# Performance work log

Hardware: AMD Instinct MI355X
Metric: run time of the kernel (lower is better)

Reference implementation:

```python
import jax, jax.numpy as jnp
import numpy as np

B, S, C = 8, 2048, 512

def setup_inputs() -> dict:
    key = jax.random.key(0)
    ks = jax.random.split(key, 7)
    s = 1.0 / np.sqrt(C)
    return {
        "x": jax.random.normal(ks[0], (B, S, C), dtype=jnp.float32),
        "Wq": jax.random.uniform(ks[1], (C, C), jnp.float32, -s, s),
        "bq": jax.random.uniform(ks[2], (C,), jnp.float32, -s, s),
        "Wk": jax.random.uniform(ks[3], (C, C), jnp.float32, -s, s),
        "bk": jax.random.uniform(ks[4], (C,), jnp.float32, -s, s),
        "Wv": jax.random.uniform(ks[5], (C, C), jnp.float32, -s, s),
        "bv": jax.random.uniform(ks[6], (C,), jnp.float32, -s, s),
    }

def reference(x, Wq, bq, Wk, bk, Wv, bv):
    # Linear projections (torch Linear: x @ W.T + b)
    q = jnp.einsum('bsc,dc->bsd', x, Wq) + bq
    k = jnp.einsum('bsc,dc->bsd', x, Wk) + bk
    v = jnp.einsum('bsc,dc->bsd', x, Wv) + bv
    # NOTE: original code computes dk but never scales by 1/sqrt(dk)
    scores = jnp.einsum('bqd,bkd->bqk', q, k)          # [B,S,S]
    attn = jax.nn.softmax(scores, axis=-1)
    out = jnp.einsum('bqk,bkd->bqd', attn, v)
    return out + x
```

## Files before the change

### kernel.cpp

```cpp
#include <hip/hip_runtime.h>
#include <hip/hip_bf16.h>


typedef __bf16 bf16_t;
typedef bf16_t bf16x8 __attribute__((ext_vector_type(8)));
typedef float floatx4 __attribute__((ext_vector_type(4)));

#define MFMA16(a, b, c) __builtin_amdgcn_mfma_f32_16x16x32_bf16((a), (b), (c), 0, 0, 0)
#define FLASH_LDS 140800

__device__ __forceinline__ void gload16(const void* g, void* l) {
    __builtin_amdgcn_global_load_lds((const __attribute__((address_space(1))) void*)g,
                                     (__attribute__((address_space(3))) void*)l, 16, 0, 0);
}

__device__ __forceinline__ float wave16_sum(float v) {
    v += __shfl_xor(v, 1);
    v += __shfl_xor(v, 2);
    v += __shfl_xor(v, 4);
    v += __shfl_xor(v, 8);
    return v;
}

__global__ void convert_in(const float* __restrict__ X,
                           const float* __restrict__ Wq, const float* __restrict__ Wk,
                           const float* __restrict__ Wv, const float* __restrict__ bq,
                           const float* __restrict__ bk, const float* __restrict__ bv,
                           bf16_t* __restrict__ Xb, bf16_t* __restrict__ Wb,
                           float* __restrict__ biasc) {
    int bid = blockIdx.x, tid = threadIdx.x;
    if (bid < 4096) {
        size_t e0 = ((size_t)bid * 256 + tid) * 8;
        float4 f0 = *(const float4*)(X + e0);
        float4 f1 = *(const float4*)(X + e0 + 4);
        bf16x8 o;
        o[0] = (bf16_t)f0.x; o[1] = (bf16_t)f0.y; o[2] = (bf16_t)f0.z; o[3] = (bf16_t)f0.w;
        o[4] = (bf16_t)f1.x; o[5] = (bf16_t)f1.y; o[6] = (bf16_t)f1.z; o[7] = (bf16_t)f1.w;
        *(bf16x8*)(Xb + e0) = o;
    } else {
        int idx = (bid - 4096) * 256 + tid;
        int e0 = idx * 4;
        int row = e0 >> 9, c = e0 & 511;
        const float* src;
        if (row < 512)       src = Wq + row * 512;
        else if (row < 1024) src = Wk + (row - 512) * 512;
        else                 src = Wv + (row - 1024) * 512;
        float4 v = *(const float4*)(src + c);
        Wb[e0 + 0] = (bf16_t)v.x;
        Wb[e0 + 1] = (bf16_t)v.y;
        Wb[e0 + 2] = (bf16_t)v.z;
        Wb[e0 + 3] = (bf16_t)v.w;
        if (idx < 1536) {
            float b;
            if (idx < 512)       b = bq[idx];
            else if (idx < 1024) b = bk[idx - 512];
            else                 b = bv[idx - 1024];
            biasc[idx] = b;
        }
    }
}

__global__ __launch_bounds__(256, 2)
void qkv_gemm(const bf16_t* __restrict__ Xb, const bf16_t* __restrict__ Wb,
              const float* __restrict__ biasc, bf16_t* __restrict__ Q,
              bf16_t* __restrict__ K, bf16_t* __restrict__ Vt) {
    __shared__ int4 smem4[2560];
    char* As = (char*)smem4;
    char* Bs = (char*)smem4 + 16384;
    char* Vtile = (char*)smem4;

    const int tid = threadIdx.x;
    const int l = tid & 63, w = tid >> 6;
    const int lane16 = l & 15, lq = l >> 4;
    const int klo = lane16 & 7;
    const int m0 = (blockIdx.x & 127) << 7;
    const int n0 = (blockIdx.x >> 7) << 7;
    const int wm = (w >> 1) << 6, wn = (w & 1) << 6;
    const int srow = l >> 3;
    const int sc8 = (l & 7) ^ srow;

    floatx4 acc[4][4];
#pragma unroll
    for (int a = 0; a < 4; ++a)
#pragma unroll
        for (int bb = 0; bb < 4; ++bb) acc[a][bb] = (floatx4){0.f, 0.f, 0.f, 0.f};

    for (int it = 0; it < 8; ++it) {
        __syncthreads();
#pragma unroll
        for (int j = 0; j < 4; ++j) {
            int seg = j * 4 + w;
            int row = seg * 8 + srow;
            gload16(Xb + (size_t)(m0 + row) * 512 + it * 64 + sc8 * 8, As + seg * 1024);
            gload16(Wb + (size_t)(n0 + row) * 512 + it * 64 + sc8 * 8, Bs + seg * 1024);
        }
        __syncthreads();
#pragma unroll
        for (int kst = 0; kst < 2; ++kst) {
            bf16x8 afr[4], bfr[4];
#pragma unroll
            for (int mt = 0; mt < 4; ++mt)
                afr[mt] = *(const bf16x8*)(As + (wm + mt * 16 + lane16) * 128 +
                                           ((kst * 4 + lq) ^ klo) * 16);
#pragma unroll
            for (int nt = 0; nt < 4; ++nt)
                bfr[nt] = *(const bf16x8*)(Bs + (wn + nt * 16 + lane16) * 128 +
                                           ((kst * 4 + lq) ^ klo) * 16);
#pragma unroll
            for (int mt = 0; mt < 4; ++mt)
#pragma unroll
                for (int nt = 0; nt < 4; ++nt)
                    acc[mt][nt] = MFMA16(afr[mt], bfr[nt], acc[mt][nt]);
        }
    }

    float bias_v[4];
#pragma unroll
    for (int nt = 0; nt < 4; ++nt) bias_v[nt] = biasc[n0 + wn + nt * 16 + lane16];

    if (n0 < 1024) {
        bf16_t* Dst = (n0 < 512) ? Q : K;
        const int coff = (n0 < 512 ? n0 : n0 - 512) + wn;
#pragma unroll
        for (int mt = 0; mt < 4; ++mt)
#pragma unroll
            for (int nt = 0; nt < 4; ++nt)
#pragma unroll
                for (int i = 0; i < 4; ++i) {
                    int rowM = m0 + wm + mt * 16 + lq * 4 + i;
                    Dst[(size_t)rowM * 512 + coff + nt * 16 + lane16] =
                        (bf16_t)(acc[mt][nt][i] + bias_v[nt]);
                }
    } else {
        __syncthreads();
#pragma unroll
        for (int mt = 0; mt < 4; ++mt)
#pragma unroll
            for (int nt = 0; nt < 4; ++nt)
#pragma unroll
                for (int i = 0; i < 4; ++i) {
                    int dl = wn + nt * 16 + lane16;
                    int sl = wm + mt * 16 + lq * 4 + i;
                    *(bf16_t*)(Vtile + dl * 264 + sl * 2) =
                        (bf16_t)(acc[mt][nt][i] + bias_v[nt]);
                }
        __syncthreads();
        const int bb = m0 >> 11, s0 = m0 & 2047, dbase = n0 - 1024;
#pragma unroll
        for (int j = 0; j < 8; ++j) {
            int slot = j * 256 + tid;
            int dd = slot >> 4, c = slot & 15;
            *(int4*)(Vt + (size_t)(bb * 512 + dbase + dd) * 2048 + s0 + c * 8) =
                *(const int4*)(Vtile + dd * 264 + c * 16);
        }
    }
}

__global__ __launch_bounds__(512, 2)
void flash_attn_v3(const bf16_t* __restrict__ Q, const bf16_t* __restrict__ K,
                   const bf16_t* __restrict__ Vt, const float* __restrict__ X,
                   float* __restrict__ Out) {
    extern __shared__ char smem[];
    char* Ks = smem;
    char* Vs = smem + 65536;
    char* Ps = smem + 131072;
    float* lpart = (float*)(smem + 140288);

    const int tid = threadIdx.x;
    const int l = tid & 63, w = tid >> 6;
    const int lane16 = l & 15, lq = l >> 4;
    const int qg = w >> 1, h = w & 1;
    const int dbase = w << 6;
    const int b = blockIdx.x & 7;
    const int q0 = (blockIdx.x >> 3) << 6;

    const bf16_t* Kbase = K + (size_t)b * 2048 * 512;
    const bf16_t* Vbase = Vt + (size_t)b * 512 * 2048;

#pragma unroll
    for (int j = 0; j < 8; ++j) {
        int seg = j * 8 + w;
        int c = (l & ~7) | ((l & 7) ^ (seg & 7));
        gload16(Kbase + (size_t)seg * 512 + c * 8, Ks + seg * 1024);
    }

    bf16x8 qf[16];
    const bf16_t* Qrow = Q + (size_t)(b * 2048 + q0 + qg * 16 + lane16) * 512 + lq * 8;
#pragma unroll
    for (int kst = 0; kst < 16; ++kst) qf[kst] = *(const bf16x8*)(Qrow + kst * 32);

    floatx4 o[16];
#pragma unroll
    for (int t = 0; t < 16; ++t) o[t] = (floatx4){0.f, 0.f, 0.f, 0.f};
    float lsum[4] = {0.f, 0.f, 0.f, 0.f};
    const float L2E = 1.4426950408889634f;

    __syncthreads();

    for (int kt = 0; kt < 32; ++kt) {
        {
            const bf16_t* Vsrc = Vbase + kt * 64;
#pragma unroll
            for (int j = 0; j < 8; ++j) {
                int seg = j * 8 + w;
                int d = seg * 8 + (l >> 3);
                int c = (l & 7) ^ (l >> 3);
                gload16(Vsrc + (size_t)d * 2048 + c * 8, Vs + seg * 1024);
            }
        }
        floatx4 scA[2], scB[2];
#pragma unroll
        for (int g = 0; g < 2; ++g) {
            scA[g] = (floatx4){0.f, 0.f, 0.f, 0.f};
            scB[g] = (floatx4){0.f, 0.f, 0.f, 0.f};
        }
#pragma unroll
        for (int kst = 0; kst < 16; kst += 2) {
#pragma unroll
            for (int g = 0; g < 2; ++g) {
                int key = h * 32 + g * 16 + lane16;
                int i0 = kst * 4 + lq;
                int i1 = i0 + 4;
                int p0 = (i0 & ~7) | ((i0 & 7) ^ (key & 7));
                int p1 = (i1 & ~7) | ((i1 & 7) ^ (key & 7));
                bf16x8 kb0 = *(const bf16x8*)(Ks + key * 1024 + p0 * 16);
                bf16x8 kb1 = *(const bf16x8*)(Ks + key * 1024 + p1 * 16);
                scA[g] = MFMA16(qf[kst], kb0, scA[g]);
                scB[g] = MFMA16(qf[kst + 1], kb1, scB[g]);
            }
        }
#pragma unroll
        for (int g = 0; g < 2; ++g) {
            int keyc = h * 32 + g * 16 + lane16;
#pragma unroll
            for (int i = 0; i < 4; ++i) {
                float p = __builtin_exp2f((scA[g][i] + scB[g][i]) * L2E);
                lsum[i] += p;
                *(bf16_t*)(Ps + (qg * 16 + lq * 4 + i) * 144 + keyc * 2) = (bf16_t)p;
            }
        }
        __syncthreads();

        if (kt < 31) {
            const bf16_t* Ksrc = Kbase + (size_t)(kt + 1) * 64 * 512;
#pragma unroll
            for (int j = 0; j < 8; ++j) {
                int seg = j * 8 + w;
                int c = (l & ~7) | ((l & 7) ^ (seg & 7));
                gload16(Ksrc + (size_t)seg * 512 + c * 8, Ks + seg * 1024);
            }
        }
#pragma unroll
        for (int kk = 0; kk < 2; ++kk) {
            bf16x8 pa[4];
#pragma unroll
            for (int qgi = 0; qgi < 4; ++qgi)
                pa[qgi] = *(const bf16x8*)(Ps + (qgi * 16 + lane16) * 144 + kk * 64 + lq * 16);
#pragma unroll
            for (int dg = 0; dg < 4; ++dg) {
                int d = dbase + dg * 16 + lane16;
                int pos = (kk * 4 + lq) ^ (d & 7);
                bf16x8 vb = *(const bf16x8*)(Vs + d * 128 + pos * 16);
#pragma unroll
                for (int qgi = 0; qgi < 4; ++qgi)
                    o[qgi * 4 + dg] = MFMA16(pa[qgi], vb, o[qgi * 4 + dg]);
            }
        }
        __syncthreads();
    }

#pragma unroll
    for (int i = 0; i < 4; ++i) {
        float s = wave16_sum(lsum[i]);
        if (lane16 == 0) lpart[(qg * 16 + lq * 4 + i) * 2 + h] = s;
    }
    __syncthreads();

#pragma unroll
    for (int qgi = 0; qgi < 4; ++qgi) {
        float rinv[4];
#pragma unroll
        for (int i = 0; i < 4; ++i) {
            int row = qgi * 16 + lq * 4 + i;
            rinv[i] = 1.0f / (lpart[row * 2] + lpart[row * 2 + 1]);
        }
#pragma unroll
        for (int dg = 0; dg < 4; ++dg) {
            int d = dbase + dg * 16 + lane16;
#pragma unroll
            for (int i = 0; i < 4; ++i) {
                int row = q0 + qgi * 16 + lq * 4 + i;
                size_t g = (size_t)(b * 2048 + row) * 512 + d;
                Out[g] = o[qgi * 4 + dg][i] * rinv[i] + X[g];
            }
        }
    }
}

extern "C" void kernel_launch(void* const* d_in, const int* in_sizes, int n_in,
                              void* d_out, int out_size, void* d_ws, size_t ws_size,
                              hipStream_t stream) {
    const float* x  = (const float*)d_in[0];
    const float* Wq = (const float*)d_in[1];
    const float* bq = (const float*)d_in[2];
    const float* Wk = (const float*)d_in[3];
    const float* bk = (const float*)d_in[4];
    const float* Wv = (const float*)d_in[5];
    const float* bv = (const float*)d_in[6];
    float* out = (float*)d_out;
    char* ws = (char*)d_ws;

    bf16_t* Wb    = (bf16_t*)(ws);
    float*  biasc = (float*)(ws + 1572864);
    bf16_t* Xb    = (bf16_t*)(ws + 1579008);
    bf16_t* Qb    = (bf16_t*)(ws + 18356224);
    bf16_t* Kb    = (bf16_t*)(ws + 35133440);
    bf16_t* Vt    = (bf16_t*)(ws + 51910656);

    convert_in<<<4864, 256, 0, stream>>>(x, Wq, Wk, Wv, bq, bk, bv, Xb, Wb, biasc);
    qkv_gemm<<<1536, 256, 0, stream>>>(Xb, Wb, biasc, Qb, Kb, Vt);

    hipFuncSetAttribute(reinterpret_cast<const void*>(flash_attn_v3),
                        hipFuncAttributeMaxDynamicSharedMemorySize, FLASH_LDS);
    flash_attn_v3<<<256, 512, FLASH_LDS, stream>>>(Qb, Kb, Vt, x, out);
}
```

Baseline: 228.8 us.

## Software-pipeline attention loop: double-buffer K and P, load V directly to registers

Restructures the flash-attention loop so K tiles are double-buffered in LDS and prefetched one iteration ahead. The P·V product for the previous key tile is deferred into the next iteration, with P double-buffered and XOR-swizzled to avoid bank conflicts. V is read straight from global memory into registers instead of staging through LDS. This cuts the loop to one barrier per iteration and overlaps QK^T with the previous PV, at the cost of more LDS and registers and uncoalesced direct V global reads.

Measured after the change: 227.0 us. No clear change (-0.8%).

```diff
diff --git a/kernel.cpp b/kernel.cpp
--- a/kernel.cpp
+++ b/kernel.cpp
@@ -7,7 +7,7 @@
 typedef float floatx4 __attribute__((ext_vector_type(4)));
 
 #define MFMA16(a, b, c) __builtin_amdgcn_mfma_f32_16x16x32_bf16((a), (b), (c), 0, 0, 0)
-#define FLASH_LDS 140800
+#define FLASH_LDS 150016
 
 __device__ __forceinline__ void gload16(const void* g, void* l) {
     __builtin_amdgcn_global_load_lds((const __attribute__((address_space(1))) void*)g,
@@ -157,14 +157,11 @@
 }
 
 __global__ __launch_bounds__(512, 2)
-void flash_attn_v3(const bf16_t* __restrict__ Q, const bf16_t* __restrict__ K,
+void flash_attn_v4(const bf16_t* __restrict__ Q, const bf16_t* __restrict__ K,
                    const bf16_t* __restrict__ Vt, const float* __restrict__ X,
                    float* __restrict__ Out) {
     extern __shared__ char smem[];
-    char* Ks = smem;
-    char* Vs = smem + 65536;
-    char* Ps = smem + 131072;
-    float* lpart = (float*)(smem + 140288);
+    float* lpart = (float*)(smem + 149504);
 
     const int tid = threadIdx.x;
     const int l = tid & 63, w = tid >> 6;
@@ -181,7 +178,7 @@
     for (int j = 0; j < 8; ++j) {
         int seg = j * 8 + w;
         int c = (l & ~7) | ((l & 7) ^ (seg & 7));
-        gload16(Kbase + (size_t)seg * 512 + c * 8, Ks + seg * 1024);
+        gload16(Kbase + (size_t)seg * 512 + c * 8, smem + seg * 1024);
     }
 
     bf16x8 qf[16];
@@ -194,20 +191,37 @@
     for (int t = 0; t < 16; ++t) o[t] = (floatx4){0.f, 0.f, 0.f, 0.f};
     float lsum[4] = {0.f, 0.f, 0.f, 0.f};
     const float L2E = 1.4426950408889634f;
+    const int srow_w = qg * 16 + lq * 4;
 
     __syncthreads();
 
     for (int kt = 0; kt < 32; ++kt) {
-        {
-            const bf16_t* Vsrc = Vbase + kt * 64;
+        char* Kcur  = smem + (kt & 1) * 65536;
+        char* Pcur  = smem + 131072 + (kt & 1) * 9216;
+        char* Pprev = smem + 131072 + ((kt ^ 1) & 1) * 9216;
+
+        bf16x8 vb[8];
+        if (kt > 0) {
+            const bf16_t* Vsrc = Vbase + (kt - 1) * 64;
+#pragma unroll
+            for (int dg = 0; dg < 4; ++dg) {
+                int d = dbase + dg * 16 + lane16;
+#pragma unroll
+                for (int kk = 0; kk < 2; ++kk)
+                    vb[dg * 2 + kk] = *(const bf16x8*)(Vsrc + (size_t)d * 2048 + kk * 32 + lq * 8);
+            }
+        }
+        if (kt < 31) {
+            const bf16_t* Ksrc = Kbase + (size_t)(kt + 1) * 64 * 512;
+            char* Knext = smem + ((kt + 1) & 1) * 65536;
 #pragma unroll
             for (int j = 0; j < 8; ++j) {
                 int seg = j * 8 + w;
-                int d = seg * 8 + (l >> 3);
-                int c = (l & 7) ^ (l >> 3);
-                gload16(Vsrc + (size_t)d * 2048 + c * 8, Vs + seg * 1024);
-            }
-        }
+                int c = (l & ~7) | ((l & 7) ^ (seg & 7));
+                gload16(Ksrc + (size_t)seg * 512 + c * 8, Knext + seg * 1024);
+            }
+        }
+
         floatx4 scA[2], scB[2];
 #pragma unroll
         for (int g = 0; g < 2; ++g) {
@@ -223,8 +237,8 @@
                 int i1 = i0 + 4;
                 int p0 = (i0 & ~7) | ((i0 & 7) ^ (key & 7));
                 int p1 = (i1 & ~7) | ((i1 & 7) ^ (key & 7));
-                bf16x8 kb0 = *(const bf16x8*)(Ks + key * 1024 + p0 * 16);
-                bf16x8 kb1 = *(const bf16x8*)(Ks + key * 1024 + p1 * 16);
+                bf16x8 kb0 = *(const bf16x8*)(Kcur + key * 1024 + p0 * 16);
+                bf16x8 kb1 = *(const bf16x8*)(Kcur + key * 1024 + p1 * 16);
                 scA[g] = MFMA16(qf[kst], kb0, scA[g]);
                 scB[g] = MFMA16(qf[kst + 1], kb1, scB[g]);
             }
@@ -232,41 +246,62 @@
 #pragma unroll
         for (int g = 0; g < 2; ++g) {
             int keyc = h * 32 + g * 16 + lane16;
+            int chunk = keyc >> 3, off = keyc & 7;
 #pragma unroll
             for (int i = 0; i < 4; ++i) {
+                int row = srow_w + i;
+                int sw = chunk ^ ((row >> 2) & 7);
                 float p = __builtin_exp2f((scA[g][i] + scB[g][i]) * L2E);
                 lsum[i] += p;
-                *(bf16_t*)(Ps + (qg * 16 + lq * 4 + i) * 144 + keyc * 2) = (bf16_t)p;
-            }
-        }
-        __syncthreads();
-
-        if (kt < 31) {
-            const bf16_t* Ksrc = Kbase + (size_t)(kt + 1) * 64 * 512;
-#pragma unroll
-            for (int j = 0; j < 8; ++j) {
-                int seg = j * 8 + w;
-                int c = (l & ~7) | ((l & 7) ^ (seg & 7));
-                gload16(Ksrc + (size_t)seg * 512 + c * 8, Ks + seg * 1024);
-            }
+                *(bf16_t*)(Pcur + row * 144 + sw * 16 + off * 2) = (bf16_t)p;
+            }
+        }
+        if (kt > 0) {
+#pragma unroll
+            for (int kk = 0; kk < 2; ++kk) {
+                bf16x8 pa[4];
+#pragma unroll
+                for (int qgi = 0; qgi < 4; ++qgi) {
+                    int row = qgi * 16 + lane16;
+                    int sw = (kk * 4 + lq) ^ ((row >> 2) & 7);
+                    pa[qgi] = *(const bf16x8*)(Pprev + row * 144 + sw * 16);
+                }
+#pragma unroll
+                for (int dg = 0; dg < 4; ++dg)
+#pragma unroll
+                    for (int qgi = 0; qgi < 4; ++qgi)
+                        o[qgi * 4 + dg] = MFMA16(pa[qgi], vb[dg * 2 + kk], o[qgi * 4 + dg]);
+            }
+        }
+        __syncthreads();
+    }
+
+    {
+        char* Plast = smem + 131072 + 9216;
+        const bf16_t* Vsrc = Vbase + 31 * 64;
+        bf16x8 vb[8];
+#pragma unroll
+        for (int dg = 0; dg < 4; ++dg) {
+            int d = dbase + dg * 16 + lane16;
+#pragma unroll
+            for (int kk = 0; kk < 2; ++kk)
+                vb[dg * 2 + kk] = *(const bf16x8*)(Vsrc + (size_t)d * 2048 + kk * 32 + lq * 8);
         }
 #pragma unroll
         for (int kk = 0; kk < 2; ++kk) {
             bf16x8 pa[4];
 #pragma unroll
-            for (int qgi = 0; qgi < 4; ++qgi)
-                pa[qgi] = *(const bf16x8*)(Ps + (qgi * 16 + lane16) * 144 + kk * 64 + lq * 16);
-#pragma unroll
-            for (int dg = 0; dg < 4; ++dg) {
-                int d = dbase + dg * 16 + lane16;
-                int pos = (kk * 4 + lq) ^ (d & 7);
-                bf16x8 vb = *(const bf16x8*)(Vs + d * 128 + pos * 16);
+            for (int qgi = 0; qgi < 4; ++qgi) {
+                int row = qgi * 16 + lane16;
+                int sw = (kk * 4 + lq) ^ ((row >> 2) & 7);
+                pa[qgi] = *(const bf16x8*)(Plast + row * 144 + sw * 16);
+            }
+#pragma unroll
+            for (int dg = 0; dg < 4; ++dg)
 #pragma unroll
                 for (int qgi = 0; qgi < 4; ++qgi)
-                    o[qgi * 4 + dg] = MFMA16(pa[qgi], vb, o[qgi * 4 + dg]);
-            }
-        }
-        __syncthreads();
+                    o[qgi * 4 + dg] = MFMA16(pa[qgi], vb[dg * 2 + kk], o[qgi * 4 + dg]);
+        }
     }
 
 #pragma unroll
@@ -320,7 +355,7 @@
     convert_in<<<4864, 256, 0, stream>>>(x, Wq, Wk, Wv, bq, bk, bv, Xb, Wb, biasc);
     qkv_gemm<<<1536, 256, 0, stream>>>(Xb, Wb, biasc, Qb, Kb, Vt);
 
-    hipFuncSetAttribute(reinterpret_cast<const void*>(flash_attn_v3),
+    hipFuncSetAttribute(reinterpret_cast<const void*>(flash_attn_v4),
                         hipFuncAttributeMaxDynamicSharedMemorySize, FLASH_LDS);
-    flash_attn_v3<<<256, 512, FLASH_LDS, stream>>>(Qb, Kb, Vt, x, out);
-}
+    flash_attn_v4<<<256, 512, FLASH_LDS, stream>>>(Qb, Kb, Vt, x, out);
+}
```
